# Kernel tuning notes

Measured on AMD Instinct MI355X. Metric: run time of the kernel, lower is better.

The kernel has to match this reference:

```python
import jax, jax.numpy as jnp
import numpy as np

T, B, D, H, A = 256, 512, 128, 128, 8
RUN_COUNT = 1000

def _orth(k, shape, scale):
    w = jax.random.normal(k, shape, jnp.float32)
    q, r = jnp.linalg.qr(w)
    q = q * jnp.sign(jnp.diag(r))[None, :]
    return scale * q

def setup_inputs() -> dict:
    key = jax.random.key(0)
    ks = jax.random.split(key, 12)
    return {
        'hidden': jnp.zeros((B, H), jnp.float32),
        'obs': jax.random.normal(ks[0], (T, B, D), jnp.float32),
        'dones': (jax.random.randint(ks[1], (T, B), 0, 10) == 0),
        'mean_obs': jax.random.normal(ks[2], (D,), jnp.float32) * 0.1,
        'welford_S': jax.random.uniform(ks[3], (D,), jnp.float32) * RUN_COUNT,
        'running_count': RUN_COUNT,
        'W_emb': _orth(ks[4], (D, H), float(np.sqrt(2.0))), 'b_emb': jnp.zeros((H,), jnp.float32),
        'Wi': jax.random.normal(ks[5], (H, 3 * H), jnp.float32) / np.sqrt(H),
        'Wh': jax.random.normal(ks[6], (H, 3 * H), jnp.float32) / np.sqrt(H),
        'bh': jnp.zeros((3 * H,), jnp.float32),
        'W_act': _orth(ks[7], (H, H), 2.0), 'b_act': jnp.zeros((H,), jnp.float32),
        'W_alpha': _orth(ks[8], (H, A), 0.01), 'b_alpha': jnp.zeros((A,), jnp.float32),
        'W_beta': _orth(ks[9], (H, A), 0.01), 'b_beta': jnp.zeros((A,), jnp.float32),
    }

def _welford(M0, S0, count0, xs):
    # sequential Welford update over stacked rows, as in the original lax.scan
    def step(carry, x):
        M, S, c = carry
        c = c + 1.0
        M_new = M + (x - M) / c
        S_new = S + (x - M) * (x - M_new)
        return (M_new, S_new, c), None
    (M, S, c), _ = jax.lax.scan(step, (M0, S0, jnp.asarray(count0, jnp.float32)), xs)
    return M, S, c

def reference(hidden, obs, dones, mean_obs, welford_S, running_count,
              W_emb, b_emb, Wi, Wh, bh, W_act, b_act, W_alpha, b_alpha, W_beta, b_beta):
    # --- running-stat normalization (running_count > 0 branch) ---
    stacked = obs.reshape(-1, obs.shape[-1])  # [T*B, D]
    M, S, c = _welford(mean_obs, welford_S, running_count, stacked)
    var = S / (c - 1.0)
    obs_n = (obs - M) / (jnp.sqrt(var) + 1e-8)
    # --- embedding MLP ---
    emb = jax.nn.relu(obs_n @ W_emb + b_emb)  # [T, B, H]
    # --- GRU scan over time; precompute input-side gate projections (no input bias, flax GRUCell) ---
    xg = emb @ Wi  # [T, B, 3H]
    def gru_step(h, inp):
        x3, reset = inp
        h = jnp.where(reset[:, None], 0.0, h)  # reset carry where done
        hg = h @ Wh + bh
        xr, xz, xn = jnp.split(x3, 3, axis=-1)
        hr, hz, hn = jnp.split(hg, 3, axis=-1)
        r = jax.nn.sigmoid(xr + hr)
        z = jax.nn.sigmoid(xz + hz)
        n = jnp.tanh(xn + r * hn)
        h_new = (1.0 - z) * n + z * h
        return h_new, h_new
    h_last, ys = jax.lax.scan(gru_step, hidden, (xg, dones))  # ys: [T, B, H]
    # --- policy heads ---
    act = jax.nn.relu(ys @ W_act + b_act)
    alpha = jax.nn.softplus(act @ W_alpha + b_alpha) + 1.0
    beta = jax.nn.softplus(act @ W_beta + b_beta) + 1.0
    return h_last, alpha, beta, M, S
```

## Files before the change

### kernel.cpp

```cpp
#include <hip/hip_runtime.h>

#define T_DIM 256
#define B_DIM 512
#define D_DIM 128
#define H_DIM 128
#define A_DIM 8
#define N_ROWS (T_DIM*B_DIM)
#define NT (N_ROWS/16)
#define NWIN 8
#define WLEN 32
#define LOG2E 1.4426950408889634f

typedef __attribute__((ext_vector_type(4))) float f32x4;
typedef __attribute__((ext_vector_type(8))) short bf16x8;
typedef __attribute__((ext_vector_type(4))) short bf16x4;
typedef __attribute__((ext_vector_type(8))) _Float16 f16x8;
typedef __attribute__((ext_vector_type(4))) unsigned u32x4;
typedef __attribute__((ext_vector_type(2))) unsigned u32x2;

#define OFF_PSUM   0ull
#define OFF_PSQ    1048576ull
#define OFF_STATM  2097152ull
#define OFF_STATI  2097664ull
#define OFF_WEMB   2098176ull
#define OFF_WI     2130944ull
#define OFF_WH     2229248ull
#define OFF_WACT   2425856ull
#define OFF_WHEAD  2458624ull
#define OFF_TLO    2462720ull
#define OFF_UH     2464768ull
#define OFF_XG     4194304ull
#define OFF_YS     104857600ull

#define OUT_H      0
#define OUT_ALPHA  65536
#define OUT_BETA   1114112
#define OUT_M      2162688
#define OUT_S      2162816

__device__ inline short f2bf(float x){
  union { float f; unsigned u; } v; v.f = x;
  unsigned r = v.u + 0x7FFFu + ((v.u>>16)&1u);
  return (short)(r>>16);
}
__device__ inline float bf2f(short h){
  union { unsigned u; float f; } v; v.u = ((unsigned)(unsigned short)h)<<16; return v.f;
}

__device__ inline int swz(int row, int col){ return row*136 + col; }

__device__ inline unsigned cvtpk_bf16(float lo, float hi){
  unsigned r;
  asm("v_cvt_pk_bf16_f32 %0, %1, %2" : "=v"(r) : "v"(lo), "v"(hi));
  return r;
}

__global__ __launch_bounds__(256) void k_partial(const float* __restrict__ obs,
                                                 double* __restrict__ psum,
                                                 double* __restrict__ psq){
  int tid = threadIdx.x; int col = tid & 127; int rh = tid >> 7;
  double s = 0.0, q = 0.0;
  for (int r = blockIdx.x*2 + rh; r < N_ROWS; r += 2048){
    float v = obs[(size_t)r*D_DIM + col];
    s += (double)v; q += (double)v*(double)v;
  }
  __shared__ double ls[256], lq[256];
  ls[tid]=s; lq[tid]=q; __syncthreads();
  if (rh==0){
    psum[(size_t)blockIdx.x*128 + col] = ls[tid] + ls[tid+128];
    psq [(size_t)blockIdx.x*128 + col] = lq[tid] + lq[tid+128];
  }
}

__global__ __launch_bounds__(1024) void k_stats(const double* __restrict__ psum,
                                                const double* __restrict__ psq,
                                                const float* __restrict__ mean_obs,
                                                const float* __restrict__ welfS,
                                                const int* __restrict__ runcnt,
                                                float* __restrict__ outM, float* __restrict__ outS,
                                                float* __restrict__ wsM,  float* __restrict__ wsI){
  int tid = threadIdx.x; int col = tid & 127; int seg = tid >> 7;
  double s=0.0, q=0.0;
  for (int b=seg; b<1024; b+=8){ s += psum[(size_t)b*128+col]; q += psq[(size_t)b*128+col]; }
  __shared__ double ls[1024], lq[1024];
  ls[tid]=s; lq[tid]=q; __syncthreads();
  if (seg==0){
    for (int b=1;b<8;b++){ s += ls[b*128+col]; q += lq[b*128+col]; }
    double c0 = (double)runcnt[0];
    double Nn = (double)N_ROWS;
    double n  = c0 + Nn;
    double M0 = (double)mean_obs[col], S0 = (double)welfS[col];
    double mb = s / Nn;
    double delta = mb - M0;
    double M = M0 + delta * Nn / n;
    double M2b = q - Nn*mb*mb;
    double S = S0 + M2b + delta*delta*c0*Nn/n;
    double var = S / (n - 1.0);
    float inv = (float)(1.0/(sqrt(var)+1e-8));
    outM[col] = (float)M; outS[col] = (float)S;
    wsM[col]  = (float)M; wsI[col]  = inv;
  }
}

__global__ void k_pack_all(const float* __restrict__ W_emb, const float* __restrict__ Wi,
                           const float* __restrict__ Wh,    const float* __restrict__ W_act,
                           const float* __restrict__ W_al,  const float* __restrict__ W_be,
                           short* __restrict__ Bemb, short* __restrict__ BWi,
                           short* __restrict__ BWh,  short* __restrict__ Bact,
                           short* __restrict__ Bhead){
  int gidx = blockIdx.x*256 + threadIdx.x;
  if (gidx >= 133120) return;
  if (gidx >= 131072){
    int idx = gidx - 131072;
    int j = idx & 7, lane = (idx>>3)&63, kb = (idx>>9)&3;
    int k = kb*32 + (lane>>4)*8 + j;
    int n = lane & 15;
    float wv = (n<8) ? W_al[(size_t)k*8 + n] : W_be[(size_t)k*8 + (n-8)];
    Bhead[idx] = f2bf(wv);
    return;
  }
  const float* src; short* dst; int C; int fmt; int idx;
  if (gidx < 16384)      { src=W_emb; dst=Bemb; C=128; fmt=0; idx=gidx; }
  else if (gidx < 65536) { src=Wi;    dst=BWi;  C=384; fmt=0; idx=gidx-16384; }
  else if (gidx < 114688){ src=Wh;    dst=BWh;  C=384; fmt=1; idx=gidx-65536; }
  else                   { src=W_act; dst=Bact; C=128; fmt=0; idx=gidx-114688; }
  int j = idx & 7, lane = (idx>>3)&63, kb = (idx>>9)&3, ct = idx>>11;
  int k = kb*32 + (lane>>4)*8 + j;
  int n = ct*16 + (lane&15);
  float wv = src[(size_t)k*C + n];
  short h;
  if (fmt==0) h = f2bf(wv);
  else {
    wv *= (n < 256) ? LOG2E : (2.f*LOG2E);
    union { _Float16 hf; short s; } u; u.hf = (_Float16)wv; h = u.s;
  }
  dst[idx] = h;
}

__global__ __launch_bounds__(512) void k_sched(const unsigned char* __restrict__ dones,
                                               int* __restrict__ tlo,
                                               unsigned char* __restrict__ usehid){
  int k = blockIdx.x;
  int b = threadIdx.x;
  int t0 = 0, uh = 1;
  if (k > 0){
    for (int t = WLEN*k; t >= 0; t--){
      if (dones[(size_t)t*B_DIM + b]){ t0 = t; uh = 0; break; }
    }
  }
  usehid[k*B_DIM + b] = (unsigned char)uh;
  __shared__ int red[512];
  red[b] = t0; __syncthreads();
  if (b < 32){
    int m = red[b*16];
    #pragma unroll
    for (int i=1;i<16;i++) m = min(m, red[b*16+i]);
    tlo[k*32 + b] = m;
  }
}

__global__ __launch_bounds__(256) void k_embxg(const float* __restrict__ obs,
                                               const float* __restrict__ wsM,
                                               const float* __restrict__ wsI,
                                               const short* __restrict__ Bemb,
                                               const float* __restrict__ b_emb,
                                               const short* __restrict__ BWi,
                                               const float* __restrict__ bh,
                                               short* __restrict__ xgpk){
  int tid=threadIdx.x, w=tid>>6, lane=tid&63, q=lane>>4, l=lane&15;
  int rt = blockIdx.x*4 + w;
  int r0 = rt*16;
  __shared__ __align__(16) short L[4][16*136];
  short* Lw = &L[w][0];

  {
    int row = lane>>2, c0 = (lane&3)*32;
    const float* op = obs + (size_t)(r0+row)*D_DIM + c0;
    #pragma unroll
    for (int it=0; it<8; it++){
      f32x4 o = *(const f32x4*)(op + it*4);
      f32x4 m = *(const f32x4*)(wsM + c0 + it*4);
      f32x4 iv= *(const f32x4*)(wsI + c0 + it*4);
      bf16x4 v;
      v[0]=f2bf((o[0]-m[0])*iv[0]); v[1]=f2bf((o[1]-m[1])*iv[1]);
      v[2]=f2bf((o[2]-m[2])*iv[2]); v[3]=f2bf((o[3]-m[3])*iv[3]);
      *(bf16x4*)&Lw[swz(row, c0+it*4)] = v;
    }
  }
  asm volatile("s_waitcnt lgkmcnt(0)" ::: "memory");

  bf16x8 A[4];
  #pragma unroll
  for (int kb=0;kb<4;kb++) A[kb] = *(const bf16x8*)&Lw[swz(l, kb*32+q*8)];
  asm volatile("s_waitcnt lgkmcnt(0)" ::: "memory");

  const bf16x8* BE = (const bf16x8*)Bemb;
  #pragma unroll
  for (int ct=0; ct<8; ct++){
    f32x4 acc = {0.f,0.f,0.f,0.f};
    #pragma unroll
    for (int kb=0;kb<4;kb++)
      acc = __builtin_amdgcn_mfma_f32_16x16x32_bf16(A[kb], BE[(ct*4+kb)*64+lane], acc, 0,0,0);
    float bb = b_emb[ct*16 + l];
    #pragma unroll
    for (int r2=0;r2<4;r2++){
      float e = acc[r2] + bb; e = e>0.f ? e : 0.f;
      Lw[swz(q*4+r2, ct*16+l)] = f2bf(e);
    }
  }
  asm volatile("s_waitcnt lgkmcnt(0)" ::: "memory");

  bf16x8 A2[4];
  #pragma unroll
  for (int kb=0;kb<4;kb++) A2[kb] = *(const bf16x8*)&Lw[swz(l, kb*32+q*8)];
  asm volatile("s_waitcnt lgkmcnt(0)" ::: "memory");

  const bf16x8* BW = (const bf16x8*)BWi;
  u32x2* xg8 = (u32x2*)xgpk;
  #pragma unroll
  for (int g=0; g<3; g++){
    #pragma unroll
    for (int c8=0; c8<8; c8++){
      int ct = g*8 + c8;
      f32x4 acc = {0.f,0.f,0.f,0.f};
      #pragma unroll
      for (int kb=0;kb<4;kb++)
        acc = __builtin_amdgcn_mfma_f32_16x16x32_bf16(A2[kb], BW[(ct*4+kb)*64+lane], acc, 0,0,0);
      int col = ct*16 + l;
      float bb = (g<2) ? bh[col] : 0.f;
      float sc = (g<2) ? LOG2E : (2.f*LOG2E);
      u32x2 pv;
      pv[0] = cvtpk_bf16((acc[0]+bb)*sc, (acc[1]+bb)*sc);
      pv[1] = cvtpk_bf16((acc[2]+bb)*sc, (acc[3]+bb)*sc);
      xg8[((size_t)rt*24 + ct)*64 + lane] = pv;
    }
  }
}

#define LDB(g,kb) __builtin_bit_cast(f16x8, pw4[(((g)*8+w)*4+(kb))*64+lane])
__global__
__attribute__((amdgpu_flat_work_group_size(512,512)))
__attribute__((amdgpu_waves_per_eu(2,2)))
void k_gru(const float* __restrict__ hidden,
           const unsigned char* __restrict__ dones,
           const short* __restrict__ xgpk,
           const short* __restrict__ BWh,
           const float* __restrict__ bh,
           const int* __restrict__ tlo,
           const unsigned char* __restrict__ usehid,
           short* __restrict__ yspk,
           float* __restrict__ h_last){
  int tid=threadIdx.x, w=tid>>6, lane=tid&63, q=lane>>4, l=lane&15;
  int kk = blockIdx.x >> 5, bt = blockIdx.x & 31;
  int t_out0 = kk*WLEN;
  int t_end  = t_out0 + WLEN;
  int t_start = tlo[kk*32 + bt];

  __shared__ __align__(16) _Float16 hF[2][16*136];

  const u32x4* pw4 = (const u32x4*)BWh;
  f16x8 B00 = LDB(0,0), B01 = LDB(0,1), B02 = LDB(0,2), B03 = LDB(0,3);
  f16x8 B10 = LDB(1,0), B11 = LDB(1,1), B12 = LDB(1,2), B13 = LDB(1,3);
  f16x8 B20 = LDB(2,0), B21 = LDB(2,1), B22 = LDB(2,2), B23 = LDB(2,3);

  float bh2c = bh[2*128 + w*16 + l] * (2.f*LOG2E);

  float hv[4];
  #pragma unroll
  for (int r2=0;r2<4;r2++){
    int b = bt*16 + q*4 + r2;
    hv[r2] = usehid[kk*B_DIM + b] ? hidden[(size_t)b*H_DIM + w*16 + l] : 0.f;
  }

  const bf16x4* xgt = (const bf16x4*)xgpk + (((size_t)t_start*32 + bt)*24 + w)*64 + lane;
  const unsigned char* dnp = dones + (size_t)t_start*B_DIM + bt*16 + q*4;
  bf16x4* yst = (bf16x4*)yspk + (((size_t)t_start*32 + bt)*8 + w)*64 + lane;

  bf16x4 xr_c = xgt[0], xz_c = xgt[512], xn_c = xgt[1024];
  unsigned dn_c = *(const unsigned*)dnp;
  { int a1 = (t_start+1 < t_end) ? 1 : 0; xgt += (size_t)a1*49152; dnp += a1*B_DIM; }
  bf16x4 xr_n = xgt[0], xz_n = xgt[512], xn_n = xgt[1024];
  unsigned dn_n = *(const unsigned*)dnp;

  _Float16* hA = &hF[0][0];
  _Float16* hB = &hF[1][0];
  const int wo = q*4*136 + w*16 + l;
  const int ro = l*136 + q*8;

  for (int t = t_start; t < t_end; t++){
    #pragma unroll
    for (int r2=0;r2<4;r2++){
      float hvv = ((dn_c >> (r2*8)) & 255u) ? 0.f : hv[r2];
      hv[r2] = hvv;
      hA[wo + r2*136] = (_Float16)hvv;
    }
    asm volatile("s_waitcnt lgkmcnt(0)" ::: "memory");
    __builtin_amdgcn_s_barrier();
    asm volatile("" ::: "memory");

    int a2 = (t+2 < t_end) ? 1 : 0;
    xgt += (size_t)a2 * 49152;
    dnp += a2 * B_DIM;
    bf16x4 xr_2 = xgt[0], xz_2 = xgt[512], xn_2 = xgt[1024];
    unsigned dn_2 = *(const unsigned*)dnp;

    f16x8 A0 = *(const f16x8*)(hA + ro +  0);
    f16x8 A1 = *(const f16x8*)(hA + ro + 32);
    f16x8 A2 = *(const f16x8*)(hA + ro + 64);
    f16x8 A3 = *(const f16x8*)(hA + ro + 96);

    f32x4 acc0 = {0.f,0.f,0.f,0.f}, acc1 = {0.f,0.f,0.f,0.f}, acc2 = {0.f,0.f,0.f,0.f};
    acc0 = __builtin_amdgcn_mfma_f32_16x16x32_f16(A0, B00, acc0, 0,0,0);
    acc1 = __builtin_amdgcn_mfma_f32_16x16x32_f16(A0, B10, acc1, 0,0,0);
    acc2 = __builtin_amdgcn_mfma_f32_16x16x32_f16(A0, B20, acc2, 0,0,0);
    acc0 = __builtin_amdgcn_mfma_f32_16x16x32_f16(A1, B01, acc0, 0,0,0);
    acc1 = __builtin_amdgcn_mfma_f32_16x16x32_f16(A1, B11, acc1, 0,0,0);
    acc2 = __builtin_amdgcn_mfma_f32_16x16x32_f16(A1, B21, acc2, 0,0,0);
    acc0 = __builtin_amdgcn_mfma_f32_16x16x32_f16(A2, B02, acc0, 0,0,0);
    acc1 = __builtin_amdgcn_mfma_f32_16x16x32_f16(A2, B12, acc1, 0,0,0);
    acc2 = __builtin_amdgcn_mfma_f32_16x16x32_f16(A2, B22, acc2, 0,0,0);
    acc0 = __builtin_amdgcn_mfma_f32_16x16x32_f16(A3, B03, acc0, 0,0,0);
    acc1 = __builtin_amdgcn_mfma_f32_16x16x32_f16(A3, B13, acc1, 0,0,0);
    acc2 = __builtin_amdgcn_mfma_f32_16x16x32_f16(A3, B23, acc2, 0,0,0);

    #pragma unroll
    for (int r2=0;r2<4;r2++){
      float xr = bf2f(xr_c[r2]), xz = bf2f(xz_c[r2]), xn = bf2f(xn_c[r2]);
      float rg = __builtin_amdgcn_rcpf(1.f + __builtin_amdgcn_exp2f(-(xr + acc0[r2])));
      float zg = __builtin_amdgcn_rcpf(1.f + __builtin_amdgcn_exp2f(-(xz + acc1[r2])));
      float e2 = __builtin_amdgcn_exp2f(xn + rg*(acc2[r2] + bh2c));
      float ng = 1.f - 2.f*__builtin_amdgcn_rcpf(e2 + 1.f);
      hv[r2] = ng + zg*(hv[r2] - ng);
    }
    if (t >= t_out0){
      u32x2 pv;
      pv[0] = cvtpk_bf16(hv[0], hv[1]);
      pv[1] = cvtpk_bf16(hv[2], hv[3]);
      *(u32x2*)yst = pv;
    }
    yst += 16384;
    xr_c = xr_n; xz_c = xz_n; xn_c = xn_n; dn_c = dn_n;
    xr_n = xr_2; xz_n = xz_2; xn_n = xn_2; dn_n = dn_2;
    _Float16* tmp = hA; hA = hB; hB = tmp;
  }

  if (kk == NWIN-1){
    #pragma unroll
    for (int r2=0;r2<4;r2++)
      h_last[(size_t)(bt*16+q*4+r2)*H_DIM + w*16 + l] = hv[r2];
  }
}

__global__ __launch_bounds__(256) void k_heads(const short* __restrict__ yspk,
                                               const short* __restrict__ Bact,
                                               const float* __restrict__ b_act,
                                               const short* __restrict__ Bhead,
                                               const float* __restrict__ b_alpha,
                                               const float* __restrict__ b_beta,
                                               float* __restrict__ alpha,
                                               float* __restrict__ beta){
  int tid=threadIdx.x, w=tid>>6, lane=tid&63, q=lane>>4, l=lane&15;
  size_t rt = (size_t)blockIdx.x*4 + w;
  __shared__ __align__(16) short tl[4][16*136];
  short* Lw = &tl[w][0];
  const bf16x4* ys4 = (const bf16x4*)yspk;
  #pragma unroll
  for (int ct=0; ct<8; ct++){
    bf16x4 v = ys4[(rt*8+ct)*64+lane];
    #pragma unroll
    for (int r2=0;r2<4;r2++) Lw[swz(q*4+r2, ct*16+l)] = v[r2];
  }
  asm volatile("s_waitcnt lgkmcnt(0)" ::: "memory");
  bf16x8 A[4];
  #pragma unroll
  for (int kb=0;kb<4;kb++) A[kb] = *(const bf16x8*)&Lw[swz(l, kb*32+q*8)];
  asm volatile("s_waitcnt lgkmcnt(0)" ::: "memory");
  const bf16x8* BA = (const bf16x8*)Bact;
  #pragma unroll
  for (int ct=0;ct<8;ct++){
    f32x4 acc = {0.f,0.f,0.f,0.f};
    #pragma unroll
    for (int kb=0;kb<4;kb++)
      acc = __builtin_amdgcn_mfma_f32_16x16x32_bf16(A[kb], BA[(ct*4+kb)*64+lane], acc, 0,0,0);
    int col = ct*16 + l;
    float bb = b_act[col];
    #pragma unroll
    for (int r2=0;r2<4;r2++){
      float e = acc[r2] + bb; e = e>0.f ? e : 0.f;
      Lw[swz(q*4+r2, col)] = f2bf(e);
    }
  }
  asm volatile("s_waitcnt lgkmcnt(0)" ::: "memory");
  bf16x8 A2[4];
  #pragma unroll
  for (int kb=0;kb<4;kb++) A2[kb] = *(const bf16x8*)&Lw[swz(l, kb*32+q*8)];
  asm volatile("s_waitcnt lgkmcnt(0)" ::: "memory");
  const bf16x8* BHd = (const bf16x8*)Bhead;
  f32x4 acc = {0.f,0.f,0.f,0.f};
  #pragma unroll
  for (int kb=0;kb<4;kb++)
    acc = __builtin_amdgcn_mfma_f32_16x16x32_bf16(A2[kb], BHd[kb*64+lane], acc, 0,0,0);
  float bb = (l<8) ? b_alpha[l] : b_beta[l-8];
  float* dst = (l<8) ? alpha : beta;
  int cc = (l<8) ? l : l-8;
  #pragma unroll
  for (int r2=0;r2<4;r2++){
    float u = acc[r2] + bb;
    float e = __builtin_amdgcn_exp2f(-fabsf(u)*LOG2E);
    float sp = fmaxf(u,0.f) + 0.6931471805599453f*__builtin_amdgcn_logf(1.f + e);
    dst[(rt*16 + q*4 + r2)*8 + cc] = sp + 1.f;
  }
}

extern "C" void kernel_launch(void* const* d_in, const int* in_sizes, int n_in,
                              void* d_out, int out_size, void* d_ws, size_t ws_size,
                              hipStream_t stream){
  const float* hidden   = (const float*)d_in[0];
  const float* obs      = (const float*)d_in[1];
  const unsigned char* dones = (const unsigned char*)d_in[2];
  const float* mean_obs = (const float*)d_in[3];
  const float* welfS    = (const float*)d_in[4];
  const int*   runcnt   = (const int*)d_in[5];
  const float* W_emb = (const float*)d_in[6];
  const float* b_emb = (const float*)d_in[7];
  const float* Wi    = (const float*)d_in[8];
  const float* Wh    = (const float*)d_in[9];
  const float* bh    = (const float*)d_in[10];
  const float* W_act = (const float*)d_in[11];
  const float* b_act = (const float*)d_in[12];
  const float* W_al  = (const float*)d_in[13];
  const float* b_al  = (const float*)d_in[14];
  const float* W_be  = (const float*)d_in[15];
  const float* b_be  = (const float*)d_in[16];
  float* out = (float*)d_out;
  char*  ws  = (char*)d_ws;

  double* psum = (double*)(ws + OFF_PSUM);
  double* psq  = (double*)(ws + OFF_PSQ);
  float*  wsM  = (float*)(ws + OFF_STATM);
  float*  wsI  = (float*)(ws + OFF_STATI);
  short*  Bemb = (short*)(ws + OFF_WEMB);
  short*  BWi  = (short*)(ws + OFF_WI);
  short*  BWh  = (short*)(ws + OFF_WH);
  short*  Bact = (short*)(ws + OFF_WACT);
  short*  Bhead= (short*)(ws + OFF_WHEAD);
  int*    tlo  = (int*)(ws + OFF_TLO);
  unsigned char* uh = (unsigned char*)(ws + OFF_UH);
  short*  xgpk = (short*)(ws + OFF_XG);
  short*  yspk = (short*)(ws + OFF_YS);

  k_partial<<<1024,256,0,stream>>>(obs, psum, psq);
  k_stats<<<1,1024,0,stream>>>(psum, psq, mean_obs, welfS, runcnt,
                               out+OUT_M, out+OUT_S, wsM, wsI);
  k_sched<<<NWIN,512,0,stream>>>(dones, tlo, uh);
  k_pack_all<<<520,256,0,stream>>>(W_emb, Wi, Wh, W_act, W_al, W_be,
                                   Bemb, BWi, BWh, Bact, Bhead);
  k_embxg<<<2048,256,0,stream>>>(obs, wsM, wsI, Bemb, b_emb, BWi, bh, xgpk);
  k_gru<<<NWIN*32,512,0,stream>>>(hidden, dones, xgpk, BWh, bh, tlo, uh,
                                  yspk, out + OUT_H);
  k_heads<<<2048,256,0,stream>>>(yspk, Bact, b_act, Bhead, b_al, b_be,
                                 out + OUT_ALPHA, out + OUT_BETA);
}
```

Measured before the change: 511.3 us.

## Fuse all stages into one persistent kernel with software grid barriers

Result: slower. 682.3 us (+33.4%).

```diff
diff --git a/kernel.cpp b/kernel.cpp
--- a/kernel.cpp
+++ b/kernel.cpp
@@ -29,6 +29,7 @@
 #define OFF_WHEAD  2458624ull
 #define OFF_TLO    2462720ull
 #define OFF_UH     2464768ull
+#define OFF_BAR    3145728ull
 #define OFF_XG     4194304ull
 #define OFF_YS     104857600ull
 
@@ -46,369 +47,369 @@
 __device__ inline float bf2f(short h){
   union { unsigned u; float f; } v; v.u = ((unsigned)(unsigned short)h)<<16; return v.f;
 }
-
 __device__ inline int swz(int row, int col){ return row*136 + col; }
-
 __device__ inline unsigned cvtpk_bf16(float lo, float hi){
   unsigned r;
   asm("v_cvt_pk_bf16_f32 %0, %1, %2" : "=v"(r) : "v"(lo), "v"(hi));
   return r;
 }
 
-__global__ __launch_bounds__(256) void k_partial(const float* __restrict__ obs,
-                                                 double* __restrict__ psum,
-                                                 double* __restrict__ psq){
-  int tid = threadIdx.x; int col = tid & 127; int rh = tid >> 7;
-  double s = 0.0, q = 0.0;
-  for (int r = blockIdx.x*2 + rh; r < N_ROWS; r += 2048){
-    float v = obs[(size_t)r*D_DIM + col];
-    s += (double)v; q += (double)v*(double)v;
-  }
-  __shared__ double ls[256], lq[256];
-  ls[tid]=s; lq[tid]=q; __syncthreads();
-  if (rh==0){
-    psum[(size_t)blockIdx.x*128 + col] = ls[tid] + ls[tid+128];
-    psq [(size_t)blockIdx.x*128 + col] = lq[tid] + lq[tid+128];
-  }
-}
-
-__global__ __launch_bounds__(1024) void k_stats(const double* __restrict__ psum,
-                                                const double* __restrict__ psq,
-                                                const float* __restrict__ mean_obs,
-                                                const float* __restrict__ welfS,
-                                                const int* __restrict__ runcnt,
-                                                float* __restrict__ outM, float* __restrict__ outS,
-                                                float* __restrict__ wsM,  float* __restrict__ wsI){
-  int tid = threadIdx.x; int col = tid & 127; int seg = tid >> 7;
-  double s=0.0, q=0.0;
-  for (int b=seg; b<1024; b+=8){ s += psum[(size_t)b*128+col]; q += psq[(size_t)b*128+col]; }
-  __shared__ double ls[1024], lq[1024];
-  ls[tid]=s; lq[tid]=q; __syncthreads();
-  if (seg==0){
-    for (int b=1;b<8;b++){ s += ls[b*128+col]; q += lq[b*128+col]; }
-    double c0 = (double)runcnt[0];
-    double Nn = (double)N_ROWS;
-    double n  = c0 + Nn;
-    double M0 = (double)mean_obs[col], S0 = (double)welfS[col];
-    double mb = s / Nn;
-    double delta = mb - M0;
-    double M = M0 + delta * Nn / n;
-    double M2b = q - Nn*mb*mb;
-    double S = S0 + M2b + delta*delta*c0*Nn/n;
-    double var = S / (n - 1.0);
-    float inv = (float)(1.0/(sqrt(var)+1e-8));
-    outM[col] = (float)M; outS[col] = (float)S;
-    wsM[col]  = (float)M; wsI[col]  = inv;
-  }
-}
-
-__global__ void k_pack_all(const float* __restrict__ W_emb, const float* __restrict__ Wi,
-                           const float* __restrict__ Wh,    const float* __restrict__ W_act,
-                           const float* __restrict__ W_al,  const float* __restrict__ W_be,
-                           short* __restrict__ Bemb, short* __restrict__ BWi,
-                           short* __restrict__ BWh,  short* __restrict__ Bact,
-                           short* __restrict__ Bhead){
-  int gidx = blockIdx.x*256 + threadIdx.x;
-  if (gidx >= 133120) return;
-  if (gidx >= 131072){
-    int idx = gidx - 131072;
-    int j = idx & 7, lane = (idx>>3)&63, kb = (idx>>9)&3;
-    int k = kb*32 + (lane>>4)*8 + j;
-    int n = lane & 15;
-    float wv = (n<8) ? W_al[(size_t)k*8 + n] : W_be[(size_t)k*8 + (n-8)];
-    Bhead[idx] = f2bf(wv);
-    return;
-  }
-  const float* src; short* dst; int C; int fmt; int idx;
-  if (gidx < 16384)      { src=W_emb; dst=Bemb; C=128; fmt=0; idx=gidx; }
-  else if (gidx < 65536) { src=Wi;    dst=BWi;  C=384; fmt=0; idx=gidx-16384; }
-  else if (gidx < 114688){ src=Wh;    dst=BWh;  C=384; fmt=1; idx=gidx-65536; }
-  else                   { src=W_act; dst=Bact; C=128; fmt=0; idx=gidx-114688; }
-  int j = idx & 7, lane = (idx>>3)&63, kb = (idx>>9)&3, ct = idx>>11;
-  int k = kb*32 + (lane>>4)*8 + j;
-  int n = ct*16 + (lane&15);
-  float wv = src[(size_t)k*C + n];
-  short h;
-  if (fmt==0) h = f2bf(wv);
-  else {
-    wv *= (n < 256) ? LOG2E : (2.f*LOG2E);
-    union { _Float16 hf; short s; } u; u.hf = (_Float16)wv; h = u.s;
-  }
-  dst[idx] = h;
-}
-
-__global__ __launch_bounds__(512) void k_sched(const unsigned char* __restrict__ dones,
-                                               int* __restrict__ tlo,
-                                               unsigned char* __restrict__ usehid){
-  int k = blockIdx.x;
-  int b = threadIdx.x;
-  int t0 = 0, uh = 1;
-  if (k > 0){
-    for (int t = WLEN*k; t >= 0; t--){
-      if (dones[(size_t)t*B_DIM + b]){ t0 = t; uh = 0; break; }
-    }
-  }
-  usehid[k*B_DIM + b] = (unsigned char)uh;
-  __shared__ int red[512];
-  red[b] = t0; __syncthreads();
-  if (b < 32){
-    int m = red[b*16];
-    #pragma unroll
-    for (int i=1;i<16;i++) m = min(m, red[b*16+i]);
-    tlo[k*32 + b] = m;
-  }
-}
-
-__global__ __launch_bounds__(256) void k_embxg(const float* __restrict__ obs,
-                                               const float* __restrict__ wsM,
-                                               const float* __restrict__ wsI,
-                                               const short* __restrict__ Bemb,
-                                               const float* __restrict__ b_emb,
-                                               const short* __restrict__ BWi,
-                                               const float* __restrict__ bh,
-                                               short* __restrict__ xgpk){
-  int tid=threadIdx.x, w=tid>>6, lane=tid&63, q=lane>>4, l=lane&15;
-  int rt = blockIdx.x*4 + w;
-  int r0 = rt*16;
-  __shared__ __align__(16) short L[4][16*136];
-  short* Lw = &L[w][0];
-
-  {
-    int row = lane>>2, c0 = (lane&3)*32;
-    const float* op = obs + (size_t)(r0+row)*D_DIM + c0;
-    #pragma unroll
-    for (int it=0; it<8; it++){
-      f32x4 o = *(const f32x4*)(op + it*4);
-      f32x4 m = *(const f32x4*)(wsM + c0 + it*4);
-      f32x4 iv= *(const f32x4*)(wsI + c0 + it*4);
-      bf16x4 v;
-      v[0]=f2bf((o[0]-m[0])*iv[0]); v[1]=f2bf((o[1]-m[1])*iv[1]);
-      v[2]=f2bf((o[2]-m[2])*iv[2]); v[3]=f2bf((o[3]-m[3])*iv[3]);
-      *(bf16x4*)&Lw[swz(row, c0+it*4)] = v;
-    }
-  }
-  asm volatile("s_waitcnt lgkmcnt(0)" ::: "memory");
-
-  bf16x8 A[4];
-  #pragma unroll
-  for (int kb=0;kb<4;kb++) A[kb] = *(const bf16x8*)&Lw[swz(l, kb*32+q*8)];
-  asm volatile("s_waitcnt lgkmcnt(0)" ::: "memory");
-
-  const bf16x8* BE = (const bf16x8*)Bemb;
-  #pragma unroll
-  for (int ct=0; ct<8; ct++){
-    f32x4 acc = {0.f,0.f,0.f,0.f};
-    #pragma unroll
-    for (int kb=0;kb<4;kb++)
-      acc = __builtin_amdgcn_mfma_f32_16x16x32_bf16(A[kb], BE[(ct*4+kb)*64+lane], acc, 0,0,0);
-    float bb = b_emb[ct*16 + l];
-    #pragma unroll
-    for (int r2=0;r2<4;r2++){
-      float e = acc[r2] + bb; e = e>0.f ? e : 0.f;
-      Lw[swz(q*4+r2, ct*16+l)] = f2bf(e);
-    }
-  }
-  asm volatile("s_waitcnt lgkmcnt(0)" ::: "memory");
-
-  bf16x8 A2[4];
-  #pragma unroll
-  for (int kb=0;kb<4;kb++) A2[kb] = *(const bf16x8*)&Lw[swz(l, kb*32+q*8)];
-  asm volatile("s_waitcnt lgkmcnt(0)" ::: "memory");
-
-  const bf16x8* BW = (const bf16x8*)BWi;
-  u32x2* xg8 = (u32x2*)xgpk;
-  #pragma unroll
-  for (int g=0; g<3; g++){
-    #pragma unroll
-    for (int c8=0; c8<8; c8++){
-      int ct = g*8 + c8;
-      f32x4 acc = {0.f,0.f,0.f,0.f};
-      #pragma unroll
-      for (int kb=0;kb<4;kb++)
-        acc = __builtin_amdgcn_mfma_f32_16x16x32_bf16(A2[kb], BW[(ct*4+kb)*64+lane], acc, 0,0,0);
-      int col = ct*16 + l;
-      float bb = (g<2) ? bh[col] : 0.f;
-      float sc = (g<2) ? LOG2E : (2.f*LOG2E);
-      u32x2 pv;
-      pv[0] = cvtpk_bf16((acc[0]+bb)*sc, (acc[1]+bb)*sc);
-      pv[1] = cvtpk_bf16((acc[2]+bb)*sc, (acc[3]+bb)*sc);
-      xg8[((size_t)rt*24 + ct)*64 + lane] = pv;
-    }
-  }
-}
-
-#define LDB(g,kb) __builtin_bit_cast(f16x8, pw4[(((g)*8+w)*4+(kb))*64+lane])
+__device__ inline void gridbar(unsigned* bar, unsigned target){
+  __syncthreads();
+  if (threadIdx.x == 0){
+    __threadfence();
+    atomicAdd(bar, 1u);
+    while (atomicAdd(bar, 0u) < target) __builtin_amdgcn_s_sleep(2);
+    __threadfence();
+  }
+  __syncthreads();
+}
+
 __global__
 __attribute__((amdgpu_flat_work_group_size(512,512)))
 __attribute__((amdgpu_waves_per_eu(2,2)))
-void k_gru(const float* __restrict__ hidden,
-           const unsigned char* __restrict__ dones,
-           const short* __restrict__ xgpk,
-           const short* __restrict__ BWh,
-           const float* __restrict__ bh,
-           const int* __restrict__ tlo,
-           const unsigned char* __restrict__ usehid,
-           short* __restrict__ yspk,
-           float* __restrict__ h_last){
-  int tid=threadIdx.x, w=tid>>6, lane=tid&63, q=lane>>4, l=lane&15;
-  int kk = blockIdx.x >> 5, bt = blockIdx.x & 31;
-  int t_out0 = kk*WLEN;
-  int t_end  = t_out0 + WLEN;
-  int t_start = tlo[kk*32 + bt];
-
-  __shared__ __align__(16) _Float16 hF[2][16*136];
-
-  const u32x4* pw4 = (const u32x4*)BWh;
-  f16x8 B00 = LDB(0,0), B01 = LDB(0,1), B02 = LDB(0,2), B03 = LDB(0,3);
-  f16x8 B10 = LDB(1,0), B11 = LDB(1,1), B12 = LDB(1,2), B13 = LDB(1,3);
-  f16x8 B20 = LDB(2,0), B21 = LDB(2,1), B22 = LDB(2,2), B23 = LDB(2,3);
-
-  float bh2c = bh[2*128 + w*16 + l] * (2.f*LOG2E);
-
-  float hv[4];
-  #pragma unroll
-  for (int r2=0;r2<4;r2++){
-    int b = bt*16 + q*4 + r2;
-    hv[r2] = usehid[kk*B_DIM + b] ? hidden[(size_t)b*H_DIM + w*16 + l] : 0.f;
-  }
-
-  const bf16x4* xgt = (const bf16x4*)xgpk + (((size_t)t_start*32 + bt)*24 + w)*64 + lane;
-  const unsigned char* dnp = dones + (size_t)t_start*B_DIM + bt*16 + q*4;
-  bf16x4* yst = (bf16x4*)yspk + (((size_t)t_start*32 + bt)*8 + w)*64 + lane;
-
-  bf16x4 xr_c = xgt[0], xz_c = xgt[512], xn_c = xgt[1024];
-  unsigned dn_c = *(const unsigned*)dnp;
-  { int a1 = (t_start+1 < t_end) ? 1 : 0; xgt += (size_t)a1*49152; dnp += a1*B_DIM; }
-  bf16x4 xr_n = xgt[0], xz_n = xgt[512], xn_n = xgt[1024];
-  unsigned dn_n = *(const unsigned*)dnp;
-
-  _Float16* hA = &hF[0][0];
-  _Float16* hB = &hF[1][0];
-  const int wo = q*4*136 + w*16 + l;
-  const int ro = l*136 + q*8;
-
-  for (int t = t_start; t < t_end; t++){
+void k_mega(const float* __restrict__ obs,
+            const unsigned char* __restrict__ dones,
+            const float* __restrict__ mean_obs,
+            const float* __restrict__ welfS,
+            const int*   __restrict__ runcnt,
+            const float* __restrict__ W_emb, const float* __restrict__ b_emb,
+            const float* __restrict__ Wi,    const float* __restrict__ Wh,
+            const float* __restrict__ bh,
+            const float* __restrict__ W_act, const float* __restrict__ b_act,
+            const float* __restrict__ W_al,  const float* __restrict__ b_al,
+            const float* __restrict__ W_be,  const float* __restrict__ b_be,
+            const float* __restrict__ hidden,
+            double* __restrict__ psum, double* __restrict__ psq,
+            float* __restrict__ wsM,  float* __restrict__ wsI,
+            short* __restrict__ Bemb, short* __restrict__ BWi,
+            short* __restrict__ BWh,  short* __restrict__ Bact,
+            short* __restrict__ Bhead,
+            int* __restrict__ tlo, unsigned char* __restrict__ usehid,
+            short* __restrict__ xgpk, short* __restrict__ yspk,
+            float* __restrict__ outM, float* __restrict__ outS,
+            float* __restrict__ h_last,
+            float* __restrict__ alpha, float* __restrict__ beta,
+            unsigned* __restrict__ bar){
+  int tid = threadIdx.x, bx = blockIdx.x;
+  __shared__ __align__(16) char U[34816];
+
+  {
+    double* ls = (double*)U; double* lq = ls + 512;
+    int col = tid & 127, rh = tid >> 7;
+    double s = 0.0, q = 0.0;
+    for (int r = bx*4 + rh; r < N_ROWS; r += 1024){
+      float v = obs[(size_t)r*D_DIM + col];
+      s += (double)v; q += (double)v*(double)v;
+    }
+    ls[tid] = s; lq[tid] = q; __syncthreads();
+    if (rh == 0){
+      psum[(size_t)bx*128 + col] = ls[tid] + ls[tid+128] + ls[tid+256] + ls[tid+384];
+      psq [(size_t)bx*128 + col] = lq[tid] + lq[tid+128] + lq[tid+256] + lq[tid+384];
+    }
+    __syncthreads();
+  }
+  if (bx < NWIN){
+    int* red = (int*)U;
+    int k = bx, b = tid;
+    int t0 = 0, uh = 1;
+    if (k > 0){
+      for (int t = WLEN*k; t >= 0; t--){
+        if (dones[(size_t)t*B_DIM + b]){ t0 = t; uh = 0; break; }
+      }
+    }
+    usehid[k*B_DIM + b] = (unsigned char)uh;
+    red[b] = t0; __syncthreads();
+    if (b < 32){
+      int m = red[b*16];
+      #pragma unroll
+      for (int i=1;i<16;i++) m = min(m, red[b*16+i]);
+      tlo[k*32 + b] = m;
+    }
+  }
+  for (int gidx = bx*512 + tid; gidx < 133120; gidx += 131072){
+    if (gidx >= 131072){
+      int idx = gidx - 131072;
+      int j = idx & 7, lane = (idx>>3)&63, kb = (idx>>9)&3;
+      int k = kb*32 + (lane>>4)*8 + j;
+      int n = lane & 15;
+      float wv = (n<8) ? W_al[(size_t)k*8 + n] : W_be[(size_t)k*8 + (n-8)];
+      Bhead[idx] = f2bf(wv);
+      continue;
+    }
+    const float* src; short* dst; int C; int fmt; int idx;
+    if (gidx < 16384)      { src=W_emb; dst=Bemb; C=128; fmt=0; idx=gidx; }
+    else if (gidx < 65536) { src=Wi;    dst=BWi;  C=384; fmt=0; idx=gidx-16384; }
+    else if (gidx < 114688){ src=Wh;    dst=BWh;  C=384; fmt=1; idx=gidx-65536; }
+    else                   { src=W_act; dst=Bact; C=128; fmt=0; idx=gidx-114688; }
+    int j = idx & 7, lane = (idx>>3)&63, kb = (idx>>9)&3, ct = idx>>11;
+    int k = kb*32 + (lane>>4)*8 + j;
+    int n = ct*16 + (lane&15);
+    float wv = src[(size_t)k*C + n];
+    short h;
+    if (fmt==0) h = f2bf(wv);
+    else {
+      wv *= (n < 256) ? LOG2E : (2.f*LOG2E);
+      union { _Float16 hf; short s; } u; u.hf = (_Float16)wv; h = u.s;
+    }
+    dst[idx] = h;
+  }
+  gridbar(bar, 256u*1);
+
+  if (bx < 128){
+    int c = bx;
+    double* sls = (double*)U; double* slq = sls + 256;
+    if (tid < 256){
+      sls[tid] = psum[(size_t)tid*128 + c];
+      slq[tid] = psq [(size_t)tid*128 + c];
+    }
+    __syncthreads();
+    if (tid < 128){ sls[tid] += sls[tid+128]; slq[tid] += slq[tid+128]; }
+    __syncthreads();
+    if (tid == 0){
+      double s=0.0, q=0.0;
+      for (int i=0;i<128;i++){ s += sls[i]; q += slq[i]; }
+      double c0 = (double)runcnt[0];
+      double Nn = (double)N_ROWS;
+      double n  = c0 + Nn;
+      double M0 = (double)mean_obs[c], S0 = (double)welfS[c];
+      double mb = s / Nn;
+      double delta = mb - M0;
+      double M = M0 + delta * Nn / n;
+      double M2b = q - Nn*mb*mb;
+      double S = S0 + M2b + delta*delta*c0*Nn/n;
+      double var = S / (n - 1.0);
+      float inv = (float)(1.0/(sqrt(var)+1e-8));
+      outM[c] = (float)M; outS[c] = (float)S;
+      wsM[c]  = (float)M; wsI[c]  = inv;
+    }
+  }
+  gridbar(bar, 256u*2);
+
+  {
+    int w=tid>>6, lane=tid&63, q=lane>>4, l=lane&15;
+    short* Lw = (short*)U + w*2176;
+    const bf16x8* BE = (const bf16x8*)Bemb;
+    const bf16x8* BW = (const bf16x8*)BWi;
+    u32x2* xg8 = (u32x2*)xgpk;
+    for (int tt=0; tt<4; tt++){
+      int rt = bx*32 + w*4 + tt;
+      int r0 = rt*16;
+      {
+        int row = lane>>2, c0 = (lane&3)*32;
+        const float* op = obs + (size_t)(r0+row)*D_DIM + c0;
+        #pragma unroll
+        for (int it=0; it<8; it++){
+          f32x4 o = *(const f32x4*)(op + it*4);
+          f32x4 m = *(const f32x4*)(wsM + c0 + it*4);
+          f32x4 iv= *(const f32x4*)(wsI + c0 + it*4);
+          bf16x4 v;
+          v[0]=f2bf((o[0]-m[0])*iv[0]); v[1]=f2bf((o[1]-m[1])*iv[1]);
+          v[2]=f2bf((o[2]-m[2])*iv[2]); v[3]=f2bf((o[3]-m[3])*iv[3]);
+          *(bf16x4*)&Lw[swz(row, c0+it*4)] = v;
+        }
+      }
+      asm volatile("s_waitcnt lgkmcnt(0)" ::: "memory");
+      bf16x8 A[4];
+      #pragma unroll
+      for (int kb=0;kb<4;kb++) A[kb] = *(const bf16x8*)&Lw[swz(l, kb*32+q*8)];
+      asm volatile("s_waitcnt lgkmcnt(0)" ::: "memory");
+      #pragma unroll
+      for (int ct=0; ct<8; ct++){
+        f32x4 acc = {0.f,0.f,0.f,0.f};
+        #pragma unroll
+        for (int kb=0;kb<4;kb++)
+          acc = __builtin_amdgcn_mfma_f32_16x16x32_bf16(A[kb], BE[(ct*4+kb)*64+lane], acc, 0,0,0);
+        float bb = b_emb[ct*16 + l];
+        #pragma unroll
+        for (int r2=0;r2<4;r2++){
+          float e = acc[r2] + bb; e = e>0.f ? e : 0.f;
+          Lw[swz(q*4+r2, ct*16+l)] = f2bf(e);
+        }
+      }
+      asm volatile("s_waitcnt lgkmcnt(0)" ::: "memory");
+      bf16x8 A2[4];
+      #pragma unroll
+      for (int kb=0;kb<4;kb++) A2[kb] = *(const bf16x8*)&Lw[swz(l, kb*32+q*8)];
+      asm volatile("s_waitcnt lgkmcnt(0)" ::: "memory");
+      #pragma unroll
+      for (int g=0; g<3; g++){
+        #pragma unroll
+        for (int c8=0; c8<8; c8++){
+          int ct = g*8 + c8;
+          f32x4 acc = {0.f,0.f,0.f,0.f};
+          #pragma unroll
+          for (int kb=0;kb<4;kb++)
+            acc = __builtin_amdgcn_mfma_f32_16x16x32_bf16(A2[kb], BW[(ct*4+kb)*64+lane], acc, 0,0,0);
+          int col = ct*16 + l;
+          float bb = (g<2) ? bh[col] : 0.f;
+          float sc = (g<2) ? LOG2E : (2.f*LOG2E);
+          u32x2 pv;
+          pv[0] = cvtpk_bf16((acc[0]+bb)*sc, (acc[1]+bb)*sc);
+          pv[1] = cvtpk_bf16((acc[2]+bb)*sc, (acc[3]+bb)*sc);
+          xg8[((size_t)rt*24 + ct)*64 + lane] = pv;
+        }
+      }
+    }
+  }
+  gridbar(bar, 256u*3);
+
+  {
+    int w=tid>>6, lane=tid&63, q=lane>>4, l=lane&15;
+    int kk = bx >> 5, bt = bx & 31;
+    int t_out0 = kk*WLEN;
+    int t_end  = t_out0 + WLEN;
+    int t_start = tlo[kk*32 + bt];
+
+    const u32x4* pw4 = (const u32x4*)BWh;
+#define LDB(g,kb) __builtin_bit_cast(f16x8, pw4[(((g)*8+w)*4+(kb))*64+lane])
+    f16x8 B00 = LDB(0,0), B01 = LDB(0,1), B02 = LDB(0,2), B03 = LDB(0,3);
+    f16x8 B10 = LDB(1,0), B11 = LDB(1,1), B12 = LDB(1,2), B13 = LDB(1,3);
+    f16x8 B20 = LDB(2,0), B21 = LDB(2,1), B22 = LDB(2,2), B23 = LDB(2,3);
+#undef LDB
+
+    float bh2c = bh[2*128 + w*16 + l] * (2.f*LOG2E);
+
+    float hv[4];
     #pragma unroll
     for (int r2=0;r2<4;r2++){
-      float hvv = ((dn_c >> (r2*8)) & 255u) ? 0.f : hv[r2];
-      hv[r2] = hvv;
-      hA[wo + r2*136] = (_Float16)hvv;
-    }
-    asm volatile("s_waitcnt lgkmcnt(0)" ::: "memory");
-    __builtin_amdgcn_s_barrier();
-    asm volatile("" ::: "memory");
-
-    int a2 = (t+2 < t_end) ? 1 : 0;
-    xgt += (size_t)a2 * 49152;
-    dnp += a2 * B_DIM;
-    bf16x4 xr_2 = xgt[0], xz_2 = xgt[512], xn_2 = xgt[1024];
-    unsigned dn_2 = *(const unsigned*)dnp;
-
-    f16x8 A0 = *(const f16x8*)(hA + ro +  0);
-    f16x8 A1 = *(const f16x8*)(hA + ro + 32);
-    f16x8 A2 = *(const f16x8*)(hA + ro + 64);
-    f16x8 A3 = *(const f16x8*)(hA + ro + 96);
-
-    f32x4 acc0 = {0.f,0.f,0.f,0.f}, acc1 = {0.f,0.f,0.f,0.f}, acc2 = {0.f,0.f,0.f,0.f};
-    acc0 = __builtin_amdgcn_mfma_f32_16x16x32_f16(A0, B00, acc0, 0,0,0);
-    acc1 = __builtin_amdgcn_mfma_f32_16x16x32_f16(A0, B10, acc1, 0,0,0);
-    acc2 = __builtin_amdgcn_mfma_f32_16x16x32_f16(A0, B20, acc2, 0,0,0);
-    acc0 = __builtin_amdgcn_mfma_f32_16x16x32_f16(A1, B01, acc0, 0,0,0);
-    acc1 = __builtin_amdgcn_mfma_f32_16x16x32_f16(A1, B11, acc1, 0,0,0);
-    acc2 = __builtin_amdgcn_mfma_f32_16x16x32_f16(A1, B21, acc2, 0,0,0);
-    acc0 = __builtin_amdgcn_mfma_f32_16x16x32_f16(A2, B02, acc0, 0,0,0);
-    acc1 = __builtin_amdgcn_mfma_f32_16x16x32_f16(A2, B12, acc1, 0,0,0);
-    acc2 = __builtin_amdgcn_mfma_f32_16x16x32_f16(A2, B22, acc2, 0,0,0);
-    acc0 = __builtin_amdgcn_mfma_f32_16x16x32_f16(A3, B03, acc0, 0,0,0);
-    acc1 = __builtin_amdgcn_mfma_f32_16x16x32_f16(A3, B13, acc1, 0,0,0);
-    acc2 = __builtin_amdgcn_mfma_f32_16x16x32_f16(A3, B23, acc2, 0,0,0);
-
-    #pragma unroll
-    for (int r2=0;r2<4;r2++){
-      float xr = bf2f(xr_c[r2]), xz = bf2f(xz_c[r2]), xn = bf2f(xn_c[r2]);
-      float rg = __builtin_amdgcn_rcpf(1.f + __builtin_amdgcn_exp2f(-(xr + acc0[r2])));
-      float zg = __builtin_amdgcn_rcpf(1.f + __builtin_amdgcn_exp2f(-(xz + acc1[r2])));
-      float e2 = __builtin_amdgcn_exp2f(xn + rg*(acc2[r2] + bh2c));
-      float ng = 1.f - 2.f*__builtin_amdgcn_rcpf(e2 + 1.f);
-      hv[r2] = ng + zg*(hv[r2] - ng);
-    }
-    if (t >= t_out0){
-      u32x2 pv;
-      pv[0] = cvtpk_bf16(hv[0], hv[1]);
-      pv[1] = cvtpk_bf16(hv[2], hv[3]);
-      *(u32x2*)yst = pv;
-    }
-    yst += 16384;
-    xr_c = xr_n; xz_c = xz_n; xn_c = xn_n; dn_c = dn_n;
-    xr_n = xr_2; xz_n = xz_2; xn_n = xn_2; dn_n = dn_2;
-    _Float16* tmp = hA; hA = hB; hB = tmp;
-  }
-
-  if (kk == NWIN-1){
-    #pragma unroll
-    for (int r2=0;r2<4;r2++)
-      h_last[(size_t)(bt*16+q*4+r2)*H_DIM + w*16 + l] = hv[r2];
-  }
-}
-
-__global__ __launch_bounds__(256) void k_heads(const short* __restrict__ yspk,
-                                               const short* __restrict__ Bact,
-                                               const float* __restrict__ b_act,
-                                               const short* __restrict__ Bhead,
-                                               const float* __restrict__ b_alpha,
-                                               const float* __restrict__ b_beta,
-                                               float* __restrict__ alpha,
-                                               float* __restrict__ beta){
-  int tid=threadIdx.x, w=tid>>6, lane=tid&63, q=lane>>4, l=lane&15;
-  size_t rt = (size_t)blockIdx.x*4 + w;
-  __shared__ __align__(16) short tl[4][16*136];
-  short* Lw = &tl[w][0];
-  const bf16x4* ys4 = (const bf16x4*)yspk;
-  #pragma unroll
-  for (int ct=0; ct<8; ct++){
-    bf16x4 v = ys4[(rt*8+ct)*64+lane];
-    #pragma unroll
-    for (int r2=0;r2<4;r2++) Lw[swz(q*4+r2, ct*16+l)] = v[r2];
-  }
-  asm volatile("s_waitcnt lgkmcnt(0)" ::: "memory");
-  bf16x8 A[4];
-  #pragma unroll
-  for (int kb=0;kb<4;kb++) A[kb] = *(const bf16x8*)&Lw[swz(l, kb*32+q*8)];
-  asm volatile("s_waitcnt lgkmcnt(0)" ::: "memory");
-  const bf16x8* BA = (const bf16x8*)Bact;
-  #pragma unroll
-  for (int ct=0;ct<8;ct++){
-    f32x4 acc = {0.f,0.f,0.f,0.f};
-    #pragma unroll
-    for (int kb=0;kb<4;kb++)
-      acc = __builtin_amdgcn_mfma_f32_16x16x32_bf16(A[kb], BA[(ct*4+kb)*64+lane], acc, 0,0,0);
-    int col = ct*16 + l;
-    float bb = b_act[col];
-    #pragma unroll
-    for (int r2=0;r2<4;r2++){
-      float e = acc[r2] + bb; e = e>0.f ? e : 0.f;
-      Lw[swz(q*4+r2, col)] = f2bf(e);
-    }
-  }
-  asm volatile("s_waitcnt lgkmcnt(0)" ::: "memory");
-  bf16x8 A2[4];
-  #pragma unroll
-  for (int kb=0;kb<4;kb++) A2[kb] = *(const bf16x8*)&Lw[swz(l, kb*32+q*8)];
-  asm volatile("s_waitcnt lgkmcnt(0)" ::: "memory");
-  const bf16x8* BHd = (const bf16x8*)Bhead;
-  f32x4 acc = {0.f,0.f,0.f,0.f};
-  #pragma unroll
-  for (int kb=0;kb<4;kb++)
-    acc = __builtin_amdgcn_mfma_f32_16x16x32_bf16(A2[kb], BHd[kb*64+lane], acc, 0,0,0);
-  float bb = (l<8) ? b_alpha[l] : b_beta[l-8];
-  float* dst = (l<8) ? alpha : beta;
-  int cc = (l<8) ? l : l-8;
-  #pragma unroll
-  for (int r2=0;r2<4;r2++){
-    float u = acc[r2] + bb;
-    float e = __builtin_amdgcn_exp2f(-fabsf(u)*LOG2E);
-    float sp = fmaxf(u,0.f) + 0.6931471805599453f*__builtin_amdgcn_logf(1.f + e);
-    dst[(rt*16 + q*4 + r2)*8 + cc] = sp + 1.f;
+      int b = bt*16 + q*4 + r2;
+      hv[r2] = usehid[kk*B_DIM + b] ? hidden[(size_t)b*H_DIM + w*16 + l] : 0.f;
+    }
+
+    const bf16x4* xgt = (const bf16x4*)xgpk + (((size_t)t_start*32 + bt)*24 + w)*64 + lane;
+    const unsigned char* dnp = dones + (size_t)t_start*B_DIM + bt*16 + q*4;
+    bf16x4* yst = (bf16x4*)yspk + (((size_t)t_start*32 + bt)*8 + w)*64 + lane;
+
+    bf16x4 xr_c = xgt[0], xz_c = xgt[512], xn_c = xgt[1024];
+    unsigned dn_c = *(const unsigned*)dnp;
+    { int a1 = (t_start+1 < t_end) ? 1 : 0; xgt += (size_t)a1*49152; dnp += a1*B_DIM; }
+    bf16x4 xr_n = xgt[0], xz_n = xgt[512], xn_n = xgt[1024];
+    unsigned dn_n = *(const unsigned*)dnp;
+
+    _Float16* hA = (_Float16*)U;
+    _Float16* hB = (_Float16*)U + 2176;
+    const int wo = q*4*136 + w*16 + l;
+    const int ro = l*136 + q*8;
+
+    for (int t = t_start; t < t_end; t++){
+      #pragma unroll
+      for (int r2=0;r2<4;r2++){
+        float hvv = ((dn_c >> (r2*8)) & 255u) ? 0.f : hv[r2];
+        hv[r2] = hvv;
+        hA[wo + r2*136] = (_Float16)hvv;
+      }
+      asm volatile("s_waitcnt lgkmcnt(0)" ::: "memory");
+      __builtin_amdgcn_s_barrier();
+      asm volatile("" ::: "memory");
+
+      int a2 = (t+2 < t_end) ? 1 : 0;
+      xgt += (size_t)a2 * 49152;
+      dnp += a2 * B_DIM;
+      bf16x4 xr_2 = xgt[0], xz_2 = xgt[512], xn_2 = xgt[1024];
+      unsigned dn_2 = *(const unsigned*)dnp;
+
+      f16x8 A0 = *(const f16x8*)(hA + ro +  0);
+      f16x8 A1 = *(const f16x8*)(hA + ro + 32);
+      f16x8 A2 = *(const f16x8*)(hA + ro + 64);
+      f16x8 A3 = *(const f16x8*)(hA + ro + 96);
+
+      f32x4 acc0 = {0.f,0.f,0.f,0.f}, acc1 = {0.f,0.f,0.f,0.f}, acc2 = {0.f,0.f,0.f,0.f};
+      acc0 = __builtin_amdgcn_mfma_f32_16x16x32_f16(A0, B00, acc0, 0,0,0);
+      acc1 = __builtin_amdgcn_mfma_f32_16x16x32_f16(A0, B10, acc1, 0,0,0);
+      acc2 = __builtin_amdgcn_mfma_f32_16x16x32_f16(A0, B20, acc2, 0,0,0);
+      acc0 = __builtin_amdgcn_mfma_f32_16x16x32_f16(A1, B01, acc0, 0,0,0);
+      acc1 = __builtin_amdgcn_mfma_f32_16x16x32_f16(A1, B11, acc1, 0,0,0);
+      acc2 = __builtin_amdgcn_mfma_f32_16x16x32_f16(A1, B21, acc2, 0,0,0);
+      acc0 = __builtin_amdgcn_mfma_f32_16x16x32_f16(A2, B02, acc0, 0,0,0);
+      acc1 = __builtin_amdgcn_mfma_f32_16x16x32_f16(A2, B12, acc1, 0,0,0);
+      acc2 = __builtin_amdgcn_mfma_f32_16x16x32_f16(A2, B22, acc2, 0,0,0);
+      acc0 = __builtin_amdgcn_mfma_f32_16x16x32_f16(A3, B03, acc0, 0,0,0);
+      acc1 = __builtin_amdgcn_mfma_f32_16x16x32_f16(A3, B13, acc1, 0,0,0);
+      acc2 = __builtin_amdgcn_mfma_f32_16x16x32_f16(A3, B23, acc2, 0,0,0);
+
+      #pragma unroll
+      for (int r2=0;r2<4;r2++){
+        float xr = bf2f(xr_c[r2]), xz = bf2f(xz_c[r2]), xn = bf2f(xn_c[r2]);
+        float rg = __builtin_amdgcn_rcpf(1.f + __builtin_amdgcn_exp2f(-(xr + acc0[r2])));
+        float zg = __builtin_amdgcn_rcpf(1.f + __builtin_amdgcn_exp2f(-(xz + acc1[r2])));
+        float e2 = __builtin_amdgcn_exp2f(xn + rg*(acc2[r2] + bh2c));
+        float ng = 1.f - 2.f*__builtin_amdgcn_rcpf(e2 + 1.f);
+        hv[r2] = ng + zg*(hv[r2] - ng);
+      }
+      if (t >= t_out0){
+        u32x2 pv;
+        pv[0] = cvtpk_bf16(hv[0], hv[1]);
+        pv[1] = cvtpk_bf16(hv[2], hv[3]);
+        *(u32x2*)yst = pv;
+      }
+      yst += 16384;
+      xr_c = xr_n; xz_c = xz_n; xn_c = xn_n; dn_c = dn_n;
+      xr_n = xr_2; xz_n = xz_2; xn_n = xn_2; dn_n = dn_2;
+      _Float16* tmp = hA; hA = hB; hB = tmp;
+    }
+
+    if (kk == NWIN-1){
+      #pragma unroll
+      for (int r2=0;r2<4;r2++)
+        h_last[(size_t)(bt*16+q*4+r2)*H_DIM + w*16 + l] = hv[r2];
+    }
+  }
+  gridbar(bar, 256u*4);
+
+  {
+    int w=tid>>6, lane=tid&63, q=lane>>4, l=lane&15;
+    short* Lw = (short*)U + w*2176;
+    const bf16x8* BA  = (const bf16x8*)Bact;
+    const bf16x8* BHd = (const bf16x8*)Bhead;
+    const bf16x4* ys4 = (const bf16x4*)yspk;
+    for (int tt=0; tt<4; tt++){
+      size_t rt = (size_t)bx*32 + w*4 + tt;
+      #pragma unroll
+      for (int ct=0; ct<8; ct++){
+        bf16x4 v = ys4[(rt*8+ct)*64+lane];
+        #pragma unroll
+        for (int r2=0;r2<4;r2++) Lw[swz(q*4+r2, ct*16+l)] = v[r2];
+      }
+      asm volatile("s_waitcnt lgkmcnt(0)" ::: "memory");
+      bf16x8 A[4];
+      #pragma unroll
+      for (int kb=0;kb<4;kb++) A[kb] = *(const bf16x8*)&Lw[swz(l, kb*32+q*8)];
+      asm volatile("s_waitcnt lgkmcnt(0)" ::: "memory");
+      #pragma unroll
+      for (int ct=0;ct<8;ct++){
+        f32x4 acc = {0.f,0.f,0.f,0.f};
+        #pragma unroll
+        for (int kb=0;kb<4;kb++)
+          acc = __builtin_amdgcn_mfma_f32_16x16x32_bf16(A[kb], BA[(ct*4+kb)*64+lane], acc, 0,0,0);
+        int col = ct*16 + l;
+        float bb = b_act[col];
+        #pragma unroll
+        for (int r2=0;r2<4;r2++){
+          float e = acc[r2] + bb; e = e>0.f ? e : 0.f;
+          Lw[swz(q*4+r2, col)] = f2bf(e);
+        }
+      }
+      asm volatile("s_waitcnt lgkmcnt(0)" ::: "memory");
+      bf16x8 A2[4];
+      #pragma unroll
+      for (int kb=0;kb<4;kb++) A2[kb] = *(const bf16x8*)&Lw[swz(l, kb*32+q*8)];
+      asm volatile("s_waitcnt lgkmcnt(0)" ::: "memory");
+      f32x4 acc = {0.f,0.f,0.f,0.f};
+      #pragma unroll
+      for (int kb=0;kb<4;kb++)
+        acc = __builtin_amdgcn_mfma_f32_16x16x32_bf16(A2[kb], BHd[kb*64+lane], acc, 0,0,0);
+      float bb = (l<8) ? b_al[l] : b_be[l-8];
+      float* dst = (l<8) ? alpha : beta;
+      int cc = (l<8) ? l : l-8;
+      #pragma unroll
+      for (int r2=0;r2<4;r2++){
+        float u = acc[r2] + bb;
+        float e = __builtin_amdgcn_exp2f(-fabsf(u)*LOG2E);
+        float sp = fmaxf(u,0.f) + 0.6931471805599453f*__builtin_amdgcn_logf(1.f + e);
+        dst[(rt*16 + q*4 + r2)*8 + cc] = sp + 1.f;
+      }
+    }
   }
 }
 
@@ -446,18 +447,19 @@
   short*  Bhead= (short*)(ws + OFF_WHEAD);
   int*    tlo  = (int*)(ws + OFF_TLO);
   unsigned char* uh = (unsigned char*)(ws + OFF_UH);
+  unsigned* bar = (unsigned*)(ws + OFF_BAR);
   short*  xgpk = (short*)(ws + OFF_XG);
   short*  yspk = (short*)(ws + OFF_YS);
 
-  k_partial<<<1024,256,0,stream>>>(obs, psum, psq);
-  k_stats<<<1,1024,0,stream>>>(psum, psq, mean_obs, welfS, runcnt,
-                               out+OUT_M, out+OUT_S, wsM, wsI);
-  k_sched<<<NWIN,512,0,stream>>>(dones, tlo, uh);
-  k_pack_all<<<520,256,0,stream>>>(W_emb, Wi, Wh, W_act, W_al, W_be,
-                                   Bemb, BWi, BWh, Bact, Bhead);
-  k_embxg<<<2048,256,0,stream>>>(obs, wsM, wsI, Bemb, b_emb, BWi, bh, xgpk);
-  k_gru<<<NWIN*32,512,0,stream>>>(hidden, dones, xgpk, BWh, bh, tlo, uh,
-                                  yspk, out + OUT_H);
-  k_heads<<<2048,256,0,stream>>>(yspk, Bact, b_act, Bhead, b_al, b_be,
-                                 out + OUT_ALPHA, out + OUT_BETA);
-}
+  hipMemsetAsync(bar, 0, 64, stream);
+  k_mega<<<256,512,0,stream>>>(obs, dones, mean_obs, welfS, runcnt,
+                               W_emb, b_emb, Wi, Wh, bh,
+                               W_act, b_act, W_al, b_al, W_be, b_be,
+                               hidden,
+                               psum, psq, wsM, wsI,
+                               Bemb, BWi, BWh, Bact, Bhead,
+                               tlo, uh, xgpk, yspk,
+                               out+OUT_M, out+OUT_S, out+OUT_H,
+                               out+OUT_ALPHA, out+OUT_BETA,
+                               bar);
+}
```
